# Optimization experiments

Measured on AMD Instinct MI355X. Metric: run time of the kernel, lower is better.

Reference implementation:

```python
import jax, jax.numpy as jnp
import numpy as np

DIM = 1024
N_HEADS = 16
HEAD_DIM = DIM // N_HEADS


def setup_inputs() -> dict:
    key = jax.random.key(0)
    k1, k2, k3 = jax.random.split(key, 3)
    x = jax.random.normal(k1, (1, 4096, DIM), dtype=jnp.float32)
    # nn.Linear weights stored as [out, in]; y = x @ W.T
    w_qkv = jax.random.normal(k2, (3 * DIM, DIM), dtype=jnp.float32) * (DIM ** -0.5)
    w_o = jax.random.normal(k3, (DIM, DIM), dtype=jnp.float32) * (DIM ** -0.5)
    return {"x": x, "w_qkv": w_qkv, "w_o": w_o}


def reference(x, w_qkv, w_o):
    b, s, _ = x.shape
    qkv = jnp.einsum('bsd,ed->bse', x, w_qkv)  # [b, s, 3*dim]
    qkv = qkv.reshape(b, s, 3, N_HEADS, HEAD_DIM)
    qkv = jnp.transpose(qkv, (2, 0, 3, 1, 4))  # [3, b, h, s, hd]
    q, k, v = qkv[0], qkv[1], qkv[2]
    scale = HEAD_DIM ** -0.5
    scores = jnp.einsum('bhqd,bhkd->bhqk', q, k) * scale  # full O(N^2) scores
    attn = jax.nn.softmax(scores, axis=-1)
    out = jnp.einsum('bhqk,bhkd->bhqd', attn, v)
    out = jnp.transpose(out, (0, 2, 1, 3)).reshape(b, s, DIM)
    return jnp.einsum('bsd,ed->bse', out, w_o)
```

## Files before the change

kernel.cpp:

```cpp
#include <hip/hip_runtime.h>

typedef __bf16 bf16x8 __attribute__((ext_vector_type(8)));
typedef float f32x4 __attribute__((ext_vector_type(4)));
typedef unsigned short ushort_t;
typedef unsigned int uint_t;

constexpr int S = 4096, DMODEL = 1024, NH = 16, HD = 64;
#define QSCALE 0.18033688011112042f

#if __has_builtin(__builtin_amdgcn_exp2f)
#define EXP2(x) __builtin_amdgcn_exp2f(x)
#else
#define EXP2(x) exp2f(x)
#endif

__device__ inline ushort_t f2bf(float f) {
  uint_t u = __builtin_bit_cast(uint_t, f);
  u = u + 0x7FFFu + ((u >> 16) & 1u);
  return (ushort_t)(u >> 16);
}

__device__ inline ushort_t f2bf_hw(float f) {
  __bf16 h = (__bf16)f;
  return __builtin_bit_cast(ushort_t, h);
}

__device__ inline void gl2lds16(const ushort_t* g, ushort_t* l) {
  __builtin_amdgcn_global_load_lds(
      (const __attribute__((address_space(1))) unsigned int*)g,
      (__attribute__((address_space(3))) unsigned int*)l, 16, 0, 0);
}

__global__ __launch_bounds__(256) void cvt_f32_bf16(const float* __restrict__ in,
                                                    ushort_t* __restrict__ out, int n4) {
  int i = blockIdx.x * 256 + threadIdx.x;
  if (i >= n4) return;
  float4 f = reinterpret_cast<const float4*>(in)[i];
  ushort4 o;
  o.x = f2bf(f.x); o.y = f2bf(f.y); o.z = f2bf(f.z); o.w = f2bf(f.w);
  reinterpret_cast<ushort4*>(out)[i] = o;
}

template <int EPI>
__global__ __launch_bounds__(256) void gemm_bt(const ushort_t* __restrict__ A,
                                               const ushort_t* __restrict__ B,
                                               int M, int N, int K,
                                               float* __restrict__ Cf,
                                               ushort_t* __restrict__ qb,
                                               ushort_t* __restrict__ kb,
                                               ushort_t* __restrict__ vtb) {
  __shared__ ushort_t sA[128 * 64];
  __shared__ ushort_t sB[128 * 64];
  const int t = threadIdx.x;
  const int lane = t & 63, w = t >> 6;
  const int wr = w >> 1, wc = w & 1;
  const int lin = blockIdx.y * gridDim.x + blockIdx.x;
  const int cpx = (gridDim.x * gridDim.y) >> 3;
  const int swz = (lin & 7) * cpx + (lin >> 3);
  const int rA0 = (swz / gridDim.x) * 128, rB0 = (swz % gridDim.x) * 128;

  f32x4 acc[4][4];
#pragma unroll
  for (int m = 0; m < 4; ++m)
#pragma unroll
    for (int n = 0; n < 4; ++n) acc[m][n] = (f32x4){0.f, 0.f, 0.f, 0.f};

  const int srow = t >> 3;
  const int scol = (t & 7) * 8;
  const int ldsbase = w * 512;

  for (int k0 = 0; k0 < K; k0 += 64) {
#pragma unroll
    for (int i = 0; i < 4; ++i) {
      int r = i * 32 + srow;
      int kc = scol ^ ((r & 7) << 3);
      gl2lds16(&A[(size_t)(rA0 + r) * K + k0 + kc], &sA[i * 2048 + ldsbase]);
    }
#pragma unroll
    for (int i = 0; i < 4; ++i) {
      int r = i * 32 + srow;
      int kc = scol ^ ((r & 7) << 3);
      gl2lds16(&B[(size_t)(rB0 + r) * K + k0 + kc], &sB[i * 2048 + ldsbase]);
    }
    __syncthreads();
#pragma unroll
    for (int ks = 0; ks < 2; ++ks) {
      const int kk = ks * 32 + (lane >> 4) * 8;
      bf16x8 af[4], bfr[4];
#pragma unroll
      for (int m = 0; m < 4; ++m) {
        int row = wr * 64 + m * 16 + (lane & 15);
        af[m] = *(const bf16x8*)&sA[row * 64 + (kk ^ ((row & 7) << 3))];
      }
#pragma unroll
      for (int n = 0; n < 4; ++n) {
        int row = wc * 64 + n * 16 + (lane & 15);
        bfr[n] = *(const bf16x8*)&sB[row * 64 + (kk ^ ((row & 7) << 3))];
      }
#pragma unroll
      for (int m = 0; m < 4; ++m)
#pragma unroll
        for (int n = 0; n < 4; ++n)
          acc[m][n] = __builtin_amdgcn_mfma_f32_16x16x32_bf16(af[m], bfr[n], acc[m][n], 0, 0, 0);
    }
    __syncthreads();
  }

#pragma unroll
  for (int m = 0; m < 4; ++m)
#pragma unroll
    for (int n = 0; n < 4; ++n)
#pragma unroll
      for (int r = 0; r < 4; ++r) {
        int row = rA0 + wr * 64 + m * 16 + (lane >> 4) * 4 + r;
        int col = rB0 + wc * 64 + n * 16 + (lane & 15);
        float v = acc[m][n][r];
        if constexpr (EPI == 0) {
          Cf[(size_t)row * N + col] = v;
        } else {
          int t3 = col >> 10, h = (col >> 6) & 15, d = col & 63;
          if (t3 == 0)      qb[((size_t)h * S + row) * HD + d] = f2bf_hw(v * QSCALE);
          else if (t3 == 1) kb[((size_t)h * S + row) * HD + d] = f2bf_hw(v);
          else              vtb[((size_t)h * HD + d) * S + row] = f2bf_hw(v);
        }
      }
}

__global__ __launch_bounds__(256) void gemm_bt_n64(const ushort_t* __restrict__ A,
                                                   const ushort_t* __restrict__ B,
                                                   int M, int N, int K,
                                                   float* __restrict__ Cf) {
  __shared__ ushort_t sA[128 * 64];
  __shared__ ushort_t sB[64 * 64];
  const int t = threadIdx.x;
  const int lane = t & 63, w = t >> 6;
  const int wr = w >> 1, wc = w & 1;
  const int lin = blockIdx.y * gridDim.x + blockIdx.x;
  const int cpx = (gridDim.x * gridDim.y) >> 3;
  const int swz = (lin & 7) * cpx + (lin >> 3);
  const int rA0 = (swz / gridDim.x) * 128, rB0 = (swz % gridDim.x) * 64;

  f32x4 acc[4][2];
#pragma unroll
  for (int m = 0; m < 4; ++m)
#pragma unroll
    for (int n = 0; n < 2; ++n) acc[m][n] = (f32x4){0.f, 0.f, 0.f, 0.f};

  const int srow = t >> 3;
  const int scol = (t & 7) * 8;
  const int ldsbase = w * 512;

  for (int k0 = 0; k0 < K; k0 += 64) {
#pragma unroll
    for (int i = 0; i < 4; ++i) {
      int r = i * 32 + srow;
      int kc = scol ^ ((r & 7) << 3);
      gl2lds16(&A[(size_t)(rA0 + r) * K + k0 + kc], &sA[i * 2048 + ldsbase]);
    }
#pragma unroll
    for (int i = 0; i < 2; ++i) {
      int r = i * 32 + srow;
      int kc = scol ^ ((r & 7) << 3);
      gl2lds16(&B[(size_t)(rB0 + r) * K + k0 + kc], &sB[i * 2048 + ldsbase]);
    }
    __syncthreads();
#pragma unroll
    for (int ks = 0; ks < 2; ++ks) {
      const int kk = ks * 32 + (lane >> 4) * 8;
      bf16x8 af[4], bfr[2];
#pragma unroll
      for (int m = 0; m < 4; ++m) {
        int row = wr * 64 + m * 16 + (lane & 15);
        af[m] = *(const bf16x8*)&sA[row * 64 + (kk ^ ((row & 7) << 3))];
      }
#pragma unroll
      for (int n = 0; n < 2; ++n) {
        int row = wc * 32 + n * 16 + (lane & 15);
        bfr[n] = *(const bf16x8*)&sB[row * 64 + (kk ^ ((row & 7) << 3))];
      }
#pragma unroll
      for (int m = 0; m < 4; ++m)
#pragma unroll
        for (int n = 0; n < 2; ++n)
          acc[m][n] = __builtin_amdgcn_mfma_f32_16x16x32_bf16(af[m], bfr[n], acc[m][n], 0, 0, 0);
    }
    __syncthreads();
  }

#pragma unroll
  for (int m = 0; m < 4; ++m)
#pragma unroll
    for (int n = 0; n < 2; ++n)
#pragma unroll
      for (int r = 0; r < 4; ++r) {
        int row = rA0 + wr * 64 + m * 16 + (lane >> 4) * 4 + r;
        int col = rB0 + wc * 32 + n * 16 + (lane & 15);
        Cf[(size_t)row * N + col] = acc[m][n][r];
      }
}

__global__ __launch_bounds__(512) void attn_fwd(const ushort_t* __restrict__ qb,
                                                const ushort_t* __restrict__ kb,
                                                const ushort_t* __restrict__ vtb,
                                                ushort_t* __restrict__ aob) {
  __shared__ ushort_t sK[3][64 * 64];
  __shared__ ushort_t sV[3][64 * 64];
  __shared__ ushort_t sP[8][16 * 64];
  const int t = threadIdx.x, lane = t & 63, w = t >> 6;
  const int f = blockIdx.x;
  const int sidx = (f & 7) * 64 + (f >> 3);
  const int h = sidx >> 5;
  const int q0 = (sidx & 31) * 128;
  const ushort_t* qh = qb + (size_t)h * S * HD;
  const ushort_t* kh = kb + (size_t)h * S * HD;
  const ushort_t* vh = vtb + (size_t)h * HD * S;

  bf16x8 qf[2];
  {
    int qr = q0 + w * 16 + (lane & 15);
    const ushort_t* p = &qh[(size_t)qr * HD + (lane >> 4) * 8];
    qf[0] = *(const bf16x8*)p;
    qf[1] = *(const bf16x8*)(p + 32);
  }
  f32x4 acc[4];
#pragma unroll
  for (int n = 0; n < 4; ++n) acc[n] = (f32x4){0.f, 0.f, 0.f, 0.f};
  float lsum[4] = {0.f, 0.f, 0.f, 0.f};

  const int srow = t >> 3;
  const int scol = (t & 7) * 8;
  const int kc = scol ^ ((srow & 7) << 3);
  const int ldsbase = w * 512;
  const int kk0 = (lane >> 4) * 8;

  auto stage = [&](int buf, int kv0) {
    gl2lds16(&kh[(size_t)(kv0 + srow) * HD + kc], &sK[buf][ldsbase]);
    gl2lds16(&vh[(size_t)srow * S + kv0 + kc], &sV[buf][ldsbase]);
  };

  constexpr int NT = S / 64;
  stage(0, 0);
  stage(1, 64);

  for (int ti = 0; ti < NT; ++ti) {
    const int buf = ti % 3;
    if (ti < NT - 1) asm volatile("s_waitcnt vmcnt(2)" ::: "memory");
    else             asm volatile("s_waitcnt vmcnt(0)" ::: "memory");
    __builtin_amdgcn_sched_barrier(0);
    __builtin_amdgcn_s_barrier();

    if (ti + 2 < NT) stage((ti + 2) % 3, (ti + 2) * 64);

    const ushort_t* Kb = &sK[buf][0];
    const ushort_t* Vb = &sV[buf][0];

    f32x4 sc[4];
    __builtin_amdgcn_s_setprio(1);
#pragma unroll
    for (int nt = 0; nt < 4; ++nt) {
      sc[nt] = (f32x4){0.f, 0.f, 0.f, 0.f};
      int row = nt * 16 + (lane & 15);
#pragma unroll
      for (int ks = 0; ks < 2; ++ks) {
        int kk = ks * 32 + kk0;
        bf16x8 kf = *(const bf16x8*)&Kb[row * 64 + (kk ^ ((row & 7) << 3))];
        sc[nt] = __builtin_amdgcn_mfma_f32_16x16x32_bf16(qf[ks], kf, sc[nt], 0, 0, 0);
      }
    }
    __builtin_amdgcn_s_setprio(0);

    float p[4][4];
#pragma unroll
    for (int r = 0; r < 4; ++r) {
      float ps = 0.f;
#pragma unroll
      for (int nt = 0; nt < 4; ++nt) {
        float pv = EXP2(sc[nt][r]);
        p[nt][r] = pv;
        ps += pv;
      }
      lsum[r] += ps;
    }
    const int prow_base = (lane >> 4) * 4;
#pragma unroll
    for (int nt = 0; nt < 4; ++nt) {
      int col = nt * 16 + (lane & 15);
#pragma unroll
      for (int r = 0; r < 4; ++r) {
        int row = prow_base + r;
        sP[w][row * 64 + (col ^ ((row & 7) << 3))] = f2bf_hw(p[nt][r]);
      }
    }
    bf16x8 pf[2];
    {
      int row = lane & 15;
#pragma unroll
      for (int ks = 0; ks < 2; ++ks) {
        int kk = ks * 32 + kk0;
        pf[ks] = *(const bf16x8*)&sP[w][row * 64 + (kk ^ ((row & 7) << 3))];
      }
    }
    __builtin_amdgcn_s_setprio(1);
#pragma unroll
    for (int nt = 0; nt < 4; ++nt) {
      int row = nt * 16 + (lane & 15);
#pragma unroll
      for (int ks = 0; ks < 2; ++ks) {
        int kk = ks * 32 + kk0;
        bf16x8 vf = *(const bf16x8*)&Vb[row * 64 + (kk ^ ((row & 7) << 3))];
        acc[nt] = __builtin_amdgcn_mfma_f32_16x16x32_bf16(pf[ks], vf, acc[nt], 0, 0, 0);
      }
    }
    __builtin_amdgcn_s_setprio(0);
  }
  float linv[4];
#pragma unroll
  for (int r = 0; r < 4; ++r) {
    float l = lsum[r];
    l += __shfl_xor(l, 1);
    l += __shfl_xor(l, 2);
    l += __shfl_xor(l, 4);
    l += __shfl_xor(l, 8);
    linv[r] = 1.0f / l;
  }
#pragma unroll
  for (int nt = 0; nt < 4; ++nt)
#pragma unroll
    for (int r = 0; r < 4; ++r) {
      int row = q0 + w * 16 + (lane >> 4) * 4 + r;
      int col = h * HD + nt * 16 + (lane & 15);
      aob[(size_t)row * DMODEL + col] = f2bf_hw(acc[nt][r] * linv[r]);
    }
}

extern "C" void kernel_launch(void* const* d_in, const int* in_sizes, int n_in,
                              void* d_out, int out_size, void* d_ws, size_t ws_size,
                              hipStream_t stream) {
  const float* x = (const float*)d_in[0];
  const float* wqkv = (const float*)d_in[1];
  const float* wo = (const float*)d_in[2];
  float* out = (float*)d_out;
  char* ws = (char*)d_ws;
  const size_t MB = 1024ull * 1024ull;
  ushort_t* xb  = (ushort_t*)(ws);
  ushort_t* wqb = (ushort_t*)(ws + 8 * MB);
  ushort_t* wob = (ushort_t*)(ws + 14 * MB);
  ushort_t* qb  = (ushort_t*)(ws + 16 * MB);
  ushort_t* kb  = (ushort_t*)(ws + 24 * MB);
  ushort_t* vtb = (ushort_t*)(ws + 32 * MB);
  ushort_t* aob = (ushort_t*)(ws + 40 * MB);

  cvt_f32_bf16<<<(S * DMODEL / 4 + 255) / 256, 256, 0, stream>>>(x, xb, S * DMODEL / 4);
  cvt_f32_bf16<<<(3 * DMODEL * DMODEL / 4 + 255) / 256, 256, 0, stream>>>(wqkv, wqb, 3 * DMODEL * DMODEL / 4);
  cvt_f32_bf16<<<(DMODEL * DMODEL / 4 + 255) / 256, 256, 0, stream>>>(wo, wob, DMODEL * DMODEL / 4);

  dim3 g1(3 * DMODEL / 128, S / 128);
  gemm_bt<1><<<g1, 256, 0, stream>>>(xb, wqb, S, 3 * DMODEL, DMODEL, nullptr, qb, kb, vtb);

  attn_fwd<<<dim3(512), 512, 0, stream>>>(qb, kb, vtb, aob);

  dim3 g2(DMODEL / 64, S / 128);
  gemm_bt_n64<<<g2, 256, 0, stream>>>(aob, wob, S, DMODEL, DMODEL, out);
}
```

Baseline: 173.1 us.

## Split attention KV range in two with a separate combine kernel

Adds a templated KV-split path that launches twice as many attention blocks, each covering half of the key/value sequence. Each block writes unnormalized fp32 partial outputs and row sums to workspace, and a new combine kernel adds the two halves, normalizes, and writes the bf16 output. The aim is more parallelism and occupancy for the attention stage. The cost is extra fp32 global traffic, an extra kernel launch, and shallower double-buffering of K/V staging in the split path. The split path runs only when the workspace is large enough; otherwise the original kernel is used.

```diff
diff --git a/kernel.cpp b/kernel.cpp
--- a/kernel.cpp
+++ b/kernel.cpp
@@ -199,21 +199,30 @@
       }
 }
 
+template <int KVSPLIT>
 __global__ __launch_bounds__(512) void attn_fwd(const ushort_t* __restrict__ qb,
                                                 const ushort_t* __restrict__ kb,
                                                 const ushort_t* __restrict__ vtb,
-                                                ushort_t* __restrict__ aob) {
-  __shared__ ushort_t sK[3][64 * 64];
-  __shared__ ushort_t sV[3][64 * 64];
+                                                ushort_t* __restrict__ aob,
+                                                float* __restrict__ Op,
+                                                float* __restrict__ Lp) {
+  constexpr int NBUF = (KVSPLIT == 1) ? 3 : 2;
+  __shared__ ushort_t sK[NBUF][64 * 64];
+  __shared__ ushort_t sV[NBUF][64 * 64];
   __shared__ ushort_t sP[8][16 * 64];
   const int t = threadIdx.x, lane = t & 63, w = t >> 6;
   const int f = blockIdx.x;
-  const int sidx = (f & 7) * 64 + (f >> 3);
-  const int h = sidx >> 5;
-  const int q0 = (sidx & 31) * 128;
+  const int sidx = (f & 7) * (64 * KVSPLIT) + (f >> 3);
+  int h, split, q0;
+  if constexpr (KVSPLIT == 1) {
+    h = sidx >> 5; split = 0; q0 = (sidx & 31) * 128;
+  } else {
+    h = sidx >> 6; split = (sidx >> 5) & 1; q0 = (sidx & 31) * 128;
+  }
   const ushort_t* qh = qb + (size_t)h * S * HD;
   const ushort_t* kh = kb + (size_t)h * S * HD;
   const ushort_t* vh = vtb + (size_t)h * HD * S;
+  const int kvbase = split * (S / KVSPLIT);
 
   bf16x8 qf[2];
   {
@@ -234,22 +243,30 @@
   const int kk0 = (lane >> 4) * 8;
 
   auto stage = [&](int buf, int kv0) {
-    gl2lds16(&kh[(size_t)(kv0 + srow) * HD + kc], &sK[buf][ldsbase]);
-    gl2lds16(&vh[(size_t)srow * S + kv0 + kc], &sV[buf][ldsbase]);
+    gl2lds16(&kh[(size_t)(kvbase + kv0 + srow) * HD + kc], &sK[buf][ldsbase]);
+    gl2lds16(&vh[(size_t)srow * S + kvbase + kv0 + kc], &sV[buf][ldsbase]);
   };
 
-  constexpr int NT = S / 64;
+  constexpr int NT = (S / KVSPLIT) / 64;
   stage(0, 0);
-  stage(1, 64);
+  if constexpr (KVSPLIT == 1) stage(1, 64);
 
   for (int ti = 0; ti < NT; ++ti) {
-    const int buf = ti % 3;
-    if (ti < NT - 1) asm volatile("s_waitcnt vmcnt(2)" ::: "memory");
-    else             asm volatile("s_waitcnt vmcnt(0)" ::: "memory");
+    const int buf = ti % NBUF;
+    if constexpr (KVSPLIT == 1) {
+      if (ti < NT - 1) asm volatile("s_waitcnt vmcnt(2)" ::: "memory");
+      else             asm volatile("s_waitcnt vmcnt(0)" ::: "memory");
+    } else {
+      asm volatile("s_waitcnt vmcnt(0)" ::: "memory");
+    }
     __builtin_amdgcn_sched_barrier(0);
     __builtin_amdgcn_s_barrier();
 
-    if (ti + 2 < NT) stage((ti + 2) % 3, (ti + 2) * 64);
+    if constexpr (KVSPLIT == 1) {
+      if (ti + 2 < NT) stage((ti + 2) % 3, (ti + 2) * 64);
+    } else {
+      if (ti + 1 < NT) stage((ti + 1) & 1, (ti + 1) * 64);
+    }
 
     const ushort_t* Kb = &sK[buf][0];
     const ushort_t* Vb = &sV[buf][0];
@@ -313,7 +330,7 @@
     }
     __builtin_amdgcn_s_setprio(0);
   }
-  float linv[4];
+  float lred[4];
 #pragma unroll
   for (int r = 0; r < 4; ++r) {
     float l = lsum[r];
@@ -321,16 +338,54 @@
     l += __shfl_xor(l, 2);
     l += __shfl_xor(l, 4);
     l += __shfl_xor(l, 8);
-    linv[r] = 1.0f / l;
-  }
-#pragma unroll
-  for (int nt = 0; nt < 4; ++nt)
-#pragma unroll
-    for (int r = 0; r < 4; ++r) {
-      int row = q0 + w * 16 + (lane >> 4) * 4 + r;
-      int col = h * HD + nt * 16 + (lane & 15);
-      aob[(size_t)row * DMODEL + col] = f2bf_hw(acc[nt][r] * linv[r]);
-    }
+    lred[r] = l;
+  }
+  if constexpr (KVSPLIT == 1) {
+#pragma unroll
+    for (int nt = 0; nt < 4; ++nt)
+#pragma unroll
+      for (int r = 0; r < 4; ++r) {
+        int row = q0 + w * 16 + (lane >> 4) * 4 + r;
+        int col = h * HD + nt * 16 + (lane & 15);
+        aob[(size_t)row * DMODEL + col] = f2bf_hw(acc[nt][r] / lred[r]);
+      }
+  } else {
+    float* Os = Op + (size_t)split * S * DMODEL;
+#pragma unroll
+    for (int nt = 0; nt < 4; ++nt)
+#pragma unroll
+      for (int r = 0; r < 4; ++r) {
+        int row = q0 + w * 16 + (lane >> 4) * 4 + r;
+        int col = h * HD + nt * 16 + (lane & 15);
+        Os[(size_t)row * DMODEL + col] = acc[nt][r];
+      }
+    if ((lane & 15) == 0) {
+#pragma unroll
+      for (int r = 0; r < 4; ++r) {
+        int row = q0 + w * 16 + (lane >> 4) * 4 + r;
+        Lp[((size_t)split * NH + h) * S + row] = lred[r];
+      }
+    }
+  }
+}
+
+__global__ __launch_bounds__(256) void attn_combine(const float* __restrict__ Op,
+                                                    const float* __restrict__ Lp,
+                                                    ushort_t* __restrict__ aob) {
+  int i = blockIdx.x * 256 + threadIdx.x;
+  int s = i >> 8;
+  int c4 = (i & 255) * 4;
+  int h = c4 >> 6;
+  const float4 a0 = *(const float4*)&Op[(size_t)s * DMODEL + c4];
+  const float4 a1 = *(const float4*)&Op[(size_t)S * DMODEL + (size_t)s * DMODEL + c4];
+  float l = Lp[(size_t)h * S + s] + Lp[(size_t)(NH + h) * S + s];
+  float inv = 1.0f / l;
+  ushort4 o;
+  o.x = f2bf_hw((a0.x + a1.x) * inv);
+  o.y = f2bf_hw((a0.y + a1.y) * inv);
+  o.z = f2bf_hw((a0.z + a1.z) * inv);
+  o.w = f2bf_hw((a0.w + a1.w) * inv);
+  *(ushort4*)&aob[(size_t)s * DMODEL + c4] = o;
 }
 
 extern "C" void kernel_launch(void* const* d_in, const int* in_sizes, int n_in,
@@ -349,6 +404,8 @@
   ushort_t* kb  = (ushort_t*)(ws + 24 * MB);
   ushort_t* vtb = (ushort_t*)(ws + 32 * MB);
   ushort_t* aob = (ushort_t*)(ws + 40 * MB);
+  float* Op = (float*)(ws + 48 * MB);
+  float* Lp = (float*)(ws + 80 * MB);
 
   cvt_f32_bf16<<<(S * DMODEL / 4 + 255) / 256, 256, 0, stream>>>(x, xb, S * DMODEL / 4);
   cvt_f32_bf16<<<(3 * DMODEL * DMODEL / 4 + 255) / 256, 256, 0, stream>>>(wqkv, wqb, 3 * DMODEL * DMODEL / 4);
@@ -357,7 +414,12 @@
   dim3 g1(3 * DMODEL / 128, S / 128);
   gemm_bt<1><<<g1, 256, 0, stream>>>(xb, wqb, S, 3 * DMODEL, DMODEL, nullptr, qb, kb, vtb);
 
-  attn_fwd<<<dim3(512), 512, 0, stream>>>(qb, kb, vtb, aob);
+  if (ws_size >= 81 * MB) {
+    attn_fwd<2><<<dim3(1024), 512, 0, stream>>>(qb, kb, vtb, nullptr, Op, Lp);
+    attn_combine<<<dim3(S * DMODEL / 4 / 256), 256, 0, stream>>>(Op, Lp, aob);
+  } else {
+    attn_fwd<1><<<dim3(512), 512, 0, stream>>>(qb, kb, vtb, aob, nullptr, nullptr);
+  }
 
   dim3 g2(DMODEL / 64, S / 128);
   gemm_bt_n64<<<g2, 256, 0, stream>>>(aob, wob, S, DMODEL, DMODEL, out);
```

Measured after the change: 185.9 us. 1.07x slower.

## Keep attention P in registers via transposed QK MFMA; merge conversion kernels

Applied to the files above, without the earlier changes.

The attention kernel now computes S^T by swapping MFMA operands. The exponentiated probabilities then land directly in the register layout that a 16x16x16 bf16 MFMA needs as its A operand. This removes the per-wave LDS round-trip for P, along with its stores and loads, and makes the row-sum a single scalar reduction across lane groups. The PV product now uses twice as many smaller MFMAs with 8-byte V reads. Separately, the three fp32-to-bf16 conversion launches are merged into one kernel, saving launch overhead.

```diff
diff --git a/kernel.cpp b/kernel.cpp
--- a/kernel.cpp
+++ b/kernel.cpp
@@ -1,6 +1,8 @@
 #include <hip/hip_runtime.h>
 
 typedef __bf16 bf16x8 __attribute__((ext_vector_type(8)));
+typedef __bf16 bf16x4 __attribute__((ext_vector_type(4)));
+typedef short shortx4 __attribute__((ext_vector_type(4)));
 typedef float f32x4 __attribute__((ext_vector_type(4)));
 typedef unsigned short ushort_t;
 typedef unsigned int uint_t;
@@ -25,20 +27,44 @@
   return __builtin_bit_cast(ushort_t, h);
 }
 
+__device__ inline f32x4 mfma16_bf16(bf16x4 a, bf16x4 b, f32x4 c) {
+#if __has_builtin(__builtin_amdgcn_mfma_f32_16x16x16bf16_1k)
+  return __builtin_amdgcn_mfma_f32_16x16x16bf16_1k(
+      __builtin_bit_cast(shortx4, a), __builtin_bit_cast(shortx4, b), c, 0, 0, 0);
+#else
+  bf16x8 a8 = {a[0], a[1], a[2], a[3], (__bf16)0.f, (__bf16)0.f, (__bf16)0.f, (__bf16)0.f};
+  bf16x8 b8 = {b[0], b[1], b[2], b[3], (__bf16)0.f, (__bf16)0.f, (__bf16)0.f, (__bf16)0.f};
+  return __builtin_amdgcn_mfma_f32_16x16x32_bf16(a8, b8, c, 0, 0, 0);
+#endif
+}
+
 __device__ inline void gl2lds16(const ushort_t* g, ushort_t* l) {
   __builtin_amdgcn_global_load_lds(
       (const __attribute__((address_space(1))) unsigned int*)g,
       (__attribute__((address_space(3))) unsigned int*)l, 16, 0, 0);
 }
 
-__global__ __launch_bounds__(256) void cvt_f32_bf16(const float* __restrict__ in,
-                                                    ushort_t* __restrict__ out, int n4) {
+constexpr int N4_X = S * DMODEL / 4;
+constexpr int N4_WQ = 3 * DMODEL * DMODEL / 4;
+constexpr int N4_WO = DMODEL * DMODEL / 4;
+__global__ __launch_bounds__(256) void cvt_all(const float* __restrict__ x,
+                                               const float* __restrict__ wqkv,
+                                               const float* __restrict__ wo,
+                                               ushort_t* __restrict__ xb,
+                                               ushort_t* __restrict__ wqb,
+                                               ushort_t* __restrict__ wob) {
   int i = blockIdx.x * 256 + threadIdx.x;
-  if (i >= n4) return;
-  float4 f = reinterpret_cast<const float4*>(in)[i];
+  const float* src;
+  ushort_t* dst;
+  int off;
+  if (i < N4_X) { src = x; dst = xb; off = i; }
+  else if (i < N4_X + N4_WQ) { src = wqkv; dst = wqb; off = i - N4_X; }
+  else if (i < N4_X + N4_WQ + N4_WO) { src = wo; dst = wob; off = i - N4_X - N4_WQ; }
+  else return;
+  float4 f = reinterpret_cast<const float4*>(src)[off];
   ushort4 o;
   o.x = f2bf(f.x); o.y = f2bf(f.y); o.z = f2bf(f.z); o.w = f2bf(f.w);
-  reinterpret_cast<ushort4*>(out)[i] = o;
+  reinterpret_cast<ushort4*>(dst)[off] = o;
 }
 
 template <int EPI>
@@ -205,7 +231,6 @@
                                                 ushort_t* __restrict__ aob) {
   __shared__ ushort_t sK[3][64 * 64];
   __shared__ ushort_t sV[3][64 * 64];
-  __shared__ ushort_t sP[8][16 * 64];
   const int t = threadIdx.x, lane = t & 63, w = t >> 6;
   const int f = blockIdx.x;
   const int sidx = (f & 7) * 64 + (f >> 3);
@@ -215,23 +240,24 @@
   const ushort_t* kh = kb + (size_t)h * S * HD;
   const ushort_t* vh = vtb + (size_t)h * HD * S;
 
+  const int l15 = lane & 15, g = lane >> 4;
+  const int kk0 = g * 8;
+
   bf16x8 qf[2];
   {
-    int qr = q0 + w * 16 + (lane & 15);
-    const ushort_t* p = &qh[(size_t)qr * HD + (lane >> 4) * 8];
+    const ushort_t* p = &qh[(size_t)(q0 + w * 16 + l15) * HD + kk0];
     qf[0] = *(const bf16x8*)p;
     qf[1] = *(const bf16x8*)(p + 32);
   }
   f32x4 acc[4];
 #pragma unroll
   for (int n = 0; n < 4; ++n) acc[n] = (f32x4){0.f, 0.f, 0.f, 0.f};
-  float lsum[4] = {0.f, 0.f, 0.f, 0.f};
+  float lsum = 0.f;
 
   const int srow = t >> 3;
   const int scol = (t & 7) * 8;
   const int kc = scol ^ ((srow & 7) << 3);
   const int ldsbase = w * 512;
-  const int kk0 = (lane >> 4) * 8;
 
   auto stage = [&](int buf, int kv0) {
     gl2lds16(&kh[(size_t)(kv0 + srow) * HD + kc], &sK[buf][ldsbase]);
@@ -259,76 +285,54 @@
 #pragma unroll
     for (int nt = 0; nt < 4; ++nt) {
       sc[nt] = (f32x4){0.f, 0.f, 0.f, 0.f};
-      int row = nt * 16 + (lane & 15);
+      int row = nt * 16 + l15;
 #pragma unroll
       for (int ks = 0; ks < 2; ++ks) {
         int kk = ks * 32 + kk0;
         bf16x8 kf = *(const bf16x8*)&Kb[row * 64 + (kk ^ ((row & 7) << 3))];
-        sc[nt] = __builtin_amdgcn_mfma_f32_16x16x32_bf16(qf[ks], kf, sc[nt], 0, 0, 0);
+        sc[nt] = __builtin_amdgcn_mfma_f32_16x16x32_bf16(kf, qf[ks], sc[nt], 0, 0, 0);
       }
     }
     __builtin_amdgcn_s_setprio(0);
 
-    float p[4][4];
-#pragma unroll
-    for (int r = 0; r < 4; ++r) {
-      float ps = 0.f;
-#pragma unroll
-      for (int nt = 0; nt < 4; ++nt) {
-        float pv = EXP2(sc[nt][r]);
-        p[nt][r] = pv;
-        ps += pv;
-      }
-      lsum[r] += ps;
-    }
-    const int prow_base = (lane >> 4) * 4;
+    bf16x4 pfrag[4];
+    float ps = 0.f;
+#pragma unroll
+    for (int c = 0; c < 4; ++c) {
+      float p0 = EXP2(sc[c][0]), p1 = EXP2(sc[c][1]);
+      float p2 = EXP2(sc[c][2]), p3 = EXP2(sc[c][3]);
+      ps += (p0 + p1) + (p2 + p3);
+      pfrag[c] = (bf16x4){(__bf16)p0, (__bf16)p1, (__bf16)p2, (__bf16)p3};
+    }
+    lsum += ps;
+
+    __builtin_amdgcn_s_setprio(1);
 #pragma unroll
     for (int nt = 0; nt < 4; ++nt) {
-      int col = nt * 16 + (lane & 15);
-#pragma unroll
-      for (int r = 0; r < 4; ++r) {
-        int row = prow_base + r;
-        sP[w][row * 64 + (col ^ ((row & 7) << 3))] = f2bf_hw(p[nt][r]);
-      }
-    }
-    bf16x8 pf[2];
-    {
-      int row = lane & 15;
-#pragma unroll
-      for (int ks = 0; ks < 2; ++ks) {
-        int kk = ks * 32 + kk0;
-        pf[ks] = *(const bf16x8*)&sP[w][row * 64 + (kk ^ ((row & 7) << 3))];
-      }
-    }
-    __builtin_amdgcn_s_setprio(1);
-#pragma unroll
-    for (int nt = 0; nt < 4; ++nt) {
-      int row = nt * 16 + (lane & 15);
-#pragma unroll
-      for (int ks = 0; ks < 2; ++ks) {
-        int kk = ks * 32 + kk0;
-        bf16x8 vf = *(const bf16x8*)&Vb[row * 64 + (kk ^ ((row & 7) << 3))];
-        acc[nt] = __builtin_amdgcn_mfma_f32_16x16x32_bf16(pf[ks], vf, acc[nt], 0, 0, 0);
+      int row = nt * 16 + l15;
+      const int rsw = (row & 7) << 3;
+#pragma unroll
+      for (int c = 0; c < 4; ++c) {
+        int col = (c * 16 + g * 4) ^ rsw;
+        bf16x4 vf = *(const bf16x4*)&Vb[row * 64 + col];
+        acc[nt] = mfma16_bf16(pfrag[c], vf, acc[nt]);
       }
     }
     __builtin_amdgcn_s_setprio(0);
   }
+  float l = lsum;
+  l += __shfl_xor(l, 16);
+  l += __shfl_xor(l, 32);
+  float inv = 1.0f / l;
   float linv[4];
 #pragma unroll
-  for (int r = 0; r < 4; ++r) {
-    float l = lsum[r];
-    l += __shfl_xor(l, 1);
-    l += __shfl_xor(l, 2);
-    l += __shfl_xor(l, 4);
-    l += __shfl_xor(l, 8);
-    linv[r] = 1.0f / l;
-  }
+  for (int r = 0; r < 4; ++r) linv[r] = __shfl(inv, g * 4 + r);
 #pragma unroll
   for (int nt = 0; nt < 4; ++nt)
 #pragma unroll
     for (int r = 0; r < 4; ++r) {
-      int row = q0 + w * 16 + (lane >> 4) * 4 + r;
-      int col = h * HD + nt * 16 + (lane & 15);
+      int row = q0 + w * 16 + g * 4 + r;
+      int col = h * HD + nt * 16 + l15;
       aob[(size_t)row * DMODEL + col] = f2bf_hw(acc[nt][r] * linv[r]);
     }
 }
@@ -350,9 +354,7 @@
   ushort_t* vtb = (ushort_t*)(ws + 32 * MB);
   ushort_t* aob = (ushort_t*)(ws + 40 * MB);
 
-  cvt_f32_bf16<<<(S * DMODEL / 4 + 255) / 256, 256, 0, stream>>>(x, xb, S * DMODEL / 4);
-  cvt_f32_bf16<<<(3 * DMODEL * DMODEL / 4 + 255) / 256, 256, 0, stream>>>(wqkv, wqb, 3 * DMODEL * DMODEL / 4);
-  cvt_f32_bf16<<<(DMODEL * DMODEL / 4 + 255) / 256, 256, 0, stream>>>(wo, wob, DMODEL * DMODEL / 4);
+  cvt_all<<<(N4_X + N4_WQ + N4_WO + 255) / 256, 256, 0, stream>>>(x, wqkv, wo, xb, wqb, wob);
 
   dim3 g1(3 * DMODEL / 128, S / 128);
   gemm_bt<1><<<g1, 256, 0, stream>>>(xb, wqb, S, 3 * DMODEL, DMODEL, nullptr, qb, kb, vtb);
```

After: 174.1 us. Within noise of the previous version (+0.6%).
